# Kernel optimization log

Measured on AMD Instinct MI355X. Metric: run time of the kernel, lower is better.

## Reference

```python
import jax, jax.numpy as jnp
import numpy as np

B, L, D = 2, 2048, 2048
H, HKV, HD = 16, 4, 128
GROUPS = H // HKV


def _rope_tables(key):
    # standard RoPE cos/sin tables, shape (B, L, HD)
    inv_freq = 1.0 / (10000.0 ** (jnp.arange(0, HD, 2, dtype=jnp.float32) / HD))
    pos = jnp.arange(L, dtype=jnp.float32)
    freqs = pos[:, None] * inv_freq[None, :]          # (L, HD/2)
    emb = jnp.concatenate([freqs, freqs], axis=-1)    # (L, HD)
    cos = jnp.broadcast_to(jnp.cos(emb)[None], (B, L, HD))
    sin = jnp.broadcast_to(jnp.sin(emb)[None], (B, L, HD))
    return cos, sin


def setup_inputs() -> dict:
    key = jax.random.key(0)
    ks = jax.random.split(key, 5)
    x = jax.random.normal(ks[0], (B, L, D), dtype=jnp.float32)
    cos, sin = _rope_tables(ks[1])
    s = 1.0 / np.sqrt(D)
    Wq = jax.random.normal(ks[2], (D, D), dtype=jnp.float32) * s
    bq = jnp.zeros((D,), dtype=jnp.float32)
    Wkv = jax.random.normal(ks[3], (2 * HKV * HD, D), dtype=jnp.float32) * s
    bkv = jnp.zeros((2 * HKV * HD,), dtype=jnp.float32)
    Wo = jax.random.normal(ks[4], (D, D), dtype=jnp.float32) * s
    bo = jnp.zeros((D,), dtype=jnp.float32)
    return {"x": x, "cos": cos, "sin": sin, "Wq": Wq, "bq": bq,
            "Wkv": Wkv, "bkv": bkv, "Wo": Wo, "bo": bo}


def _rotate_half(t):
    t1, t2 = jnp.split(t, 2, axis=-1)
    return jnp.concatenate([-t2, t1], axis=-1)


def reference(x, cos, sin, Wq, bq, Wkv, bkv, Wo, bo):
    b, l, d = x.shape
    # QKV projections
    q = (x @ Wq.T + bq).reshape(b, l, H, HD)
    kv = (x @ Wkv.T + bkv).reshape(b, l, 2, HKV, HD)
    k, v = kv[:, :, 0], kv[:, :, 1]
    # RoPE (unsqueeze over head dim, layout B,L,H,D)
    c = cos[:, :, None, :]
    s = sin[:, :, None, :]
    q = q * c + _rotate_half(q) * s
    k = k * c + _rotate_half(k) * s
    # GQA: expand kv heads to query heads
    k = jnp.repeat(k, GROUPS, axis=2)
    v = jnp.repeat(v, GROUPS, axis=2)
    # causal attention (flash_attn_func equivalent math)
    scores = jnp.einsum("blhd,bmhd->bhlm", q, k) / jnp.sqrt(jnp.float32(HD))
    mask = jnp.tril(jnp.ones((l, l), dtype=bool))
    scores = jnp.where(mask[None, None], scores, jnp.finfo(scores.dtype).min)
    attn = jax.nn.softmax(scores, axis=-1)
    out = jnp.einsum("bhlm,bmhd->blhd", attn, v).reshape(b, l, H * HD)
    return out @ Wo.T + bo
```

## Files before the change

kernel.cpp:

```cpp
#include <hip/hip_runtime.h>
#include <hip/hip_bf16.h>
#include <cstddef>

constexpr int B = 2, L = 2048, D = 2048;
constexpr int H = 16, HKV = 4, HD = 128;
constexpr int GROUPS = H / HKV;
constexpr int KVD = 2 * HKV * HD;
constexpr int M_ROWS = B * L;
constexpr int QKVW = D + KVD;

typedef __attribute__((ext_vector_type(8))) short short8;
typedef __attribute__((ext_vector_type(4))) short s16x4;
typedef __attribute__((ext_vector_type(4))) float f32x4;

__device__ __forceinline__ short f2bf(float f) {
    union { float f; unsigned u; } v; v.f = f;
    unsigned r = v.u + 0x7FFFu + ((v.u >> 16) & 1u);
    return (short)(r >> 16);
}

__device__ __forceinline__ float fast_exp2(float x) {
#if __has_builtin(__builtin_amdgcn_exp2f)
    return __builtin_amdgcn_exp2f(x);
#else
    return exp2f(x);
#endif
}

typedef __attribute__((address_space(1))) const void cg_void;
typedef __attribute__((address_space(3))) void lds_void;
__device__ __forceinline__ void gl_lds16(const void* g, void* l) {
    __builtin_amdgcn_global_load_lds((cg_void*)g, (lds_void*)l, 16, 0, 0);
}

__global__ __launch_bounds__(256) void cast_all(
    const float* __restrict__ x, const float* __restrict__ Wq,
    const float* __restrict__ Wkv, const float* __restrict__ Wo,
    short* __restrict__ xb, short* __restrict__ wqkvb, short* __restrict__ wob)
{
    constexpr int n_x   = M_ROWS * D / 4;
    constexpr int n_wq  = D * D / 4;
    constexpr int n_wkv = KVD * D / 4;
    int i = blockIdx.x * 256 + threadIdx.x;
    const float* src; short* dst;
    if (i < n_x)                       { src = x;   dst = xb; }
    else if (i < n_x + n_wq)           { i -= n_x; src = Wq;  dst = wqkvb; }
    else if (i < n_x + n_wq + n_wkv)   { i -= n_x + n_wq; src = Wkv; dst = wqkvb + (size_t)D * D; }
    else                               { i -= n_x + n_wq + n_wkv; src = Wo; dst = wob; }
    const float4 f = ((const float4*)src)[i];
    s16x4 s;
    s[0] = f2bf(f.x); s[1] = f2bf(f.y); s[2] = f2bf(f.z); s[3] = f2bf(f.w);
    ((s16x4*)dst)[i] = s;
}

__global__ __launch_bounds__(256) void bcat(
    const float* __restrict__ bq, const float* __restrict__ bkv, float* __restrict__ o)
{
    const int i = blockIdx.x * 256 + threadIdx.x;
    o[i] = (i < D) ? bq[i] : bkv[i - D];
}

__global__ __launch_bounds__(512, 2) void gemm256(
    const short* __restrict__ Ag, const short* __restrict__ Wg,
    const float* __restrict__ bias, float* __restrict__ C,
    int M, int N, int K)
{
    __shared__ __align__(1024) char smem[131072];

    const int tid = threadIdx.x;
    const int w = tid >> 6, lane = tid & 63;
    const int quad = lane >> 4, n16 = lane & 15;
    const int wr = w >> 2, wc = w & 3;

    const int nbx = gridDim.x;
    const int nwg = nbx * gridDim.y;
    int wg = blockIdx.y * nbx + blockIdx.x;
    wg = (wg & 7) * (nwg >> 3) + (wg >> 3);
    const int bm = (wg / nbx) << 8;
    const int bn = (wg % nbx) << 8;

    const int nkt = K >> 6;

    const int sbo = n16 * 64 + ((quad * 16) ^ ((n16 & 8) << 2));

    const int srow = lane >> 2;
    const int scol = ((lane & 3) * 8) ^ (((lane >> 5) & 1) << 4);

    f32x4 acc[8][4];
#pragma unroll
    for (int i = 0; i < 8; ++i)
#pragma unroll
        for (int j = 0; j < 4; ++j)
#pragma unroll
            for (int r = 0; r < 4; ++r) acc[i][j][r] = 0.f;

    short8 afr[4][2], bfr[2][2];

#define STAGE_A(k0, cb, h)                                                     \
    { _Pragma("unroll") for (int j = 0; j < 2; ++j) {                          \
        const int s  = w + j * 8;                                              \
        const int u  = s >> 1;                                                 \
        const int rg = ((u >> 2) << 3) + ((h) << 2) + (u & 3);                 \
        const int gr = bm + (rg << 4) + srow;                                  \
        const int gc = (k0) + ((s & 1) << 5) + scol;                           \
        gl_lds16(Ag + (size_t)gr * K + gc,                                     \
                 smem + (cb) * 32768 + (h) * 16384 + (s << 10)); } }

#define STAGE_B(k0, cb, h)                                                     \
    { _Pragma("unroll") for (int j = 0; j < 2; ++j) {                          \
        const int s  = w + j * 8;                                              \
        const int u  = s >> 1;                                                 \
        const int rg = ((u >> 1) << 2) + ((h) << 1) + (u & 1);                 \
        const int gr = bn + (rg << 4) + srow;                                  \
        const int gc = (k0) + ((s & 1) << 5) + scol;                           \
        gl_lds16(Wg + (size_t)gr * K + gc,                                     \
                 smem + 65536 + (cb) * 32768 + (h) * 16384 + (s << 10)); } }

#define PHASE(CB, Q, STAGE_STMT, WAIT_STMT)                                    \
    {                                                                          \
        if (((Q) & 1) == 0) {                                                  \
            _Pragma("unroll") for (int mi2 = 0; mi2 < 4; ++mi2)                \
            _Pragma("unroll") for (int kk = 0; kk < 2; ++kk)                   \
                afr[mi2][kk] = *(const short8*)(smem + (CB) * 32768 +          \
                    ((Q) >> 1) * 16384 +                                       \
                    ((((wr * 4 + mi2) * 2) + kk) << 10) + sbo);                \
        }                                                                      \
        _Pragma("unroll") for (int ni2 = 0; ni2 < 2; ++ni2)                    \
        _Pragma("unroll") for (int kk = 0; kk < 2; ++kk)                       \
            bfr[ni2][kk] = *(const short8*)(smem + 65536 + (CB) * 32768 +      \
                ((Q) & 1) * 16384 +                                            \
                ((((wc * 2 + ni2) * 2) + kk) << 10) + sbo);                    \
        STAGE_STMT;                                                            \
        WAIT_STMT;                                                             \
        __builtin_amdgcn_s_barrier();                                          \
        asm volatile("s_waitcnt lgkmcnt(0)" ::: "memory");                     \
        __builtin_amdgcn_sched_barrier(0);                                     \
        __builtin_amdgcn_s_setprio(1);                                         \
        _Pragma("unroll") for (int mi2 = 0; mi2 < 4; ++mi2)                    \
        _Pragma("unroll") for (int ni2 = 0; ni2 < 2; ++ni2)                    \
        _Pragma("unroll") for (int kk = 0; kk < 2; ++kk)                       \
            acc[((Q) >> 1) * 4 + mi2][((Q) & 1) * 2 + ni2] =                   \
                __builtin_amdgcn_mfma_f32_16x16x32_bf16(                       \
                    afr[mi2][kk], bfr[ni2][kk],                                \
                    acc[((Q) >> 1) * 4 + mi2][((Q) & 1) * 2 + ni2], 0, 0, 0);  \
        __builtin_amdgcn_s_setprio(0);                                         \
        asm volatile("" ::: "memory");                                         \
        __builtin_amdgcn_s_barrier();                                          \
    }

#define NOP_WAIT asm volatile("" ::: "memory")

    STAGE_A(0, 0, 0);
    STAGE_B(0, 0, 0);
    STAGE_A(0, 0, 1);
    STAGE_B(0, 0, 1);
    if (nkt > 1) {
        STAGE_A(64, 1, 0);
        STAGE_B(64, 1, 0);
    }
    asm volatile("s_waitcnt vmcnt(4)" ::: "memory");
    __builtin_amdgcn_s_barrier();

    for (int t = 0; t < nkt; t += 2) {
        const int k1 = (t + 1) << 6, k2 = (t + 2) << 6, k3 = (t + 3) << 6;
        const bool g2 = (t + 2) < nkt, g3 = (t + 3) < nkt;

        PHASE(0, 0, { STAGE_A(k1, 1, 1); }, NOP_WAIT);
        PHASE(0, 1, { STAGE_B(k1, 1, 1); }, NOP_WAIT);
        PHASE(0, 2, { if (g2) STAGE_A(k2, 0, 0); }, NOP_WAIT);
        PHASE(0, 3, { if (g2) STAGE_B(k2, 0, 0); },
              { if (g2) asm volatile("s_waitcnt vmcnt(4)" ::: "memory");
                else    asm volatile("s_waitcnt vmcnt(0)" ::: "memory"); });

        PHASE(1, 0, { if (g2) STAGE_A(k2, 0, 1); }, NOP_WAIT);
        PHASE(1, 1, { if (g2) STAGE_B(k2, 0, 1); }, NOP_WAIT);
        PHASE(1, 2, { if (g3) STAGE_A(k3, 1, 0); }, NOP_WAIT);
        PHASE(1, 3, { if (g3) STAGE_B(k3, 1, 0); },
              { if (g3) asm volatile("s_waitcnt vmcnt(4)" ::: "memory");
                else    asm volatile("s_waitcnt vmcnt(0)" ::: "memory"); });
    }

#undef PHASE
#undef STAGE_A
#undef STAGE_B
#undef NOP_WAIT

#pragma unroll
    for (int mh = 0; mh < 2; ++mh)
#pragma unroll
        for (int mi2 = 0; mi2 < 4; ++mi2)
#pragma unroll
            for (int r = 0; r < 4; ++r) {
                const int row = bm + wr * 128 + mh * 64 + mi2 * 16 + quad * 4 + r;
#pragma unroll
                for (int nh = 0; nh < 2; ++nh)
#pragma unroll
                    for (int ni2 = 0; ni2 < 2; ++ni2) {
                        const int col = bn + wc * 64 + nh * 32 + ni2 * 16 + n16;
                        C[(size_t)row * N + col] =
                            acc[mh * 4 + mi2][nh * 2 + ni2][r] + bias[col];
                    }
            }
}

__global__ __launch_bounds__(256) void rope_bf(
    const float* __restrict__ qkv, const float* __restrict__ cosp,
    const float* __restrict__ sinp, short* __restrict__ qb, short* __restrict__ kb)
{
    const int row = blockIdx.x;
    const int tid = threadIdx.x;
    const int b = row / L, l = row % L;
    const float* cr = cosp + (size_t)row * HD;
    const float* sr = sinp + (size_t)row * HD;
    const float* base = qkv + (size_t)row * QKVW;

    for (int p = tid; p < H * 64; p += 256) {
        const int h = p >> 6, i = p & 63;
        const float* qr = base + h * HD;
        short* qo = qb + (size_t)row * D + h * HD;
        const float t1 = qr[i], t2 = qr[i + 64];
        qo[i]      = f2bf(t1 * cr[i]      - t2 * sr[i]);
        qo[i + 64] = f2bf(t2 * cr[i + 64] + t1 * sr[i + 64]);
    }
    {
        const int h = tid >> 6, i = tid & 63;
        const float* krow = base + D + h * HD;
        short* ko = kb + ((size_t)(b * HKV + h) * L + l) * HD;
        const float t1 = krow[i], t2 = krow[i + 64];
        ko[i]      = f2bf(t1 * cr[i]      - t2 * sr[i]);
        ko[i + 64] = f2bf(t2 * cr[i + 64] + t1 * sr[i + 64]);
    }
}

__global__ __launch_bounds__(256) void vt_kernel(
    const float* __restrict__ qkv, short* __restrict__ vt)
{
    __shared__ short T[32][72];
    const int lt = blockIdx.x, dt = blockIdx.y, bh = blockIdx.z;
    const int b = bh >> 2, hkv = bh & 3;
    const int tid = threadIdx.x;

#pragma unroll
    for (int pass = 0; pass < 2; ++pass) {
        const int ll = pass * 32 + (tid >> 3);
        const int dl = (tid & 7) * 4;
        const int l = lt * 64 + ll;
        const float4 f = *(const float4*)&qkv[
            ((size_t)(b * L + l)) * QKVW + D + HKV * HD + hkv * HD + dt * 32 + dl];
        T[dl + 0][ll] = f2bf(f.x); T[dl + 1][ll] = f2bf(f.y);
        T[dl + 2][ll] = f2bf(f.z); T[dl + 3][ll] = f2bf(f.w);
    }
    __syncthreads();
#pragma unroll
    for (int pass = 0; pass < 2; ++pass) {
        const int dl = pass * 16 + (tid >> 4);
        const int l4 = (tid & 15) * 4;
        const int d = dt * 32 + dl;
        *(s16x4*)&vt[((size_t)bh * HD + d) * L + lt * 64 + l4] = *(const s16x4*)&T[dl][l4];
    }
}

__global__ __launch_bounds__(512) void attn_mfma4(
    const short* __restrict__ qb_, const short* __restrict__ kb_,
    const short* __restrict__ vtb_, short* __restrict__ ob)
{
    __shared__ __align__(16) char smem[86016];
    short* const KsB  = (short*)smem;
    short* const VtB  = (short*)(smem + 32768);
    short* const PbB  = (short*)(smem + 65536);
    float* const Rbuf = (float*)smem;

    const int hkv = blockIdx.y, b = blockIdx.z;
    const int tid = threadIdx.x;
    const int w = tid >> 6, lane = tid & 63;
    const int quad = lane >> 4, n16 = lane & 15;
    const int h   = hkv * GROUPS + (w & 3);
    const int kh  = (w >> 2) * 32;
    const int khg = (w >> 2) * 4;

    const size_t kbase  = (size_t)(b * HKV + hkv) * L * HD;
    const size_t vtbase = (size_t)(b * HKV + hkv) * HD * L;
    const float c1 = 0.12751845f;
    const float c0 = -28.853901f;

    short8 ones;
#pragma unroll
    for (int i = 0; i < 8; ++i) ones[i] = (short)0x3F80;

    const int kr = lane >> 4;
    const int kg_sw = lane & 15;
    const int vr = lane >> 3;
    const int vg_sw = lane & 7;

    short* const myPb = PbB + w * (2 * 16 * 40);

#pragma unroll 1
    for (int phase = 0; phase < 2; ++phase) {
        const int qidx = phase ? (63 - (int)blockIdx.x) : (int)blockIdx.x;
        const int qb0 = qidx * 32;
        const int ntiles = (qidx >> 1) + 1;

        short8 qf[2][4];
#pragma unroll
        for (int rt = 0; rt < 2; ++rt)
#pragma unroll
            for (int kk = 0; kk < 4; ++kk)
                qf[rt][kk] = *(const short8*)&qb_[
                    ((size_t)(b * L + qb0 + rt * 16 + n16)) * D + h * HD + kk * 32 + quad * 8];

        f32x4 oacc[2][8], lacc[2];
#pragma unroll
        for (int rt = 0; rt < 2; ++rt) {
#pragma unroll
            for (int r = 0; r < 4; ++r) lacc[rt][r] = 0.f;
#pragma unroll
            for (int nt = 0; nt < 8; ++nt)
#pragma unroll
                for (int r = 0; r < 4; ++r) oacc[rt][nt][r] = 0.f;
        }

        __syncthreads();

        {
            const short* kg = kb_ + kbase;
            const short* vg = vtb_ + vtbase;
#pragma unroll
            for (int j = 0; j < 2; ++j) {
                const int chunk = w * 2 + j;
                const int r = chunk * 4 + kr;
                gl_lds16(kg + r * HD + (kg_sw ^ (r & 15)) * 8, KsB + chunk * 512);
            }
#pragma unroll
            for (int j = 0; j < 2; ++j) {
                const int chunk = w * 2 + j;
                const int d = chunk * 8 + vr;
                gl_lds16(vg + (size_t)d * L + (vg_sw ^ (d & 7)) * 8, VtB + chunk * 512);
            }
        }

        for (int kt = 0; kt < ntiles; ++kt) {
            const int buf = kt & 1;
            __syncthreads();

            if (kt + 1 < ntiles) {
                const short* kg = kb_ + kbase + (size_t)((kt + 1) * 64) * HD;
                const short* vg = vtb_ + vtbase + (kt + 1) * 64;
#pragma unroll
                for (int j = 0; j < 2; ++j) {
                    const int chunk = w * 2 + j;
                    const int r = chunk * 4 + kr;
                    gl_lds16(kg + r * HD + (kg_sw ^ (r & 15)) * 8,
                             KsB + (buf ^ 1) * 8192 + chunk * 512);
                }
#pragma unroll
                for (int j = 0; j < 2; ++j) {
                    const int chunk = w * 2 + j;
                    const int d = chunk * 8 + vr;
                    gl_lds16(vg + (size_t)d * L + (vg_sw ^ (d & 7)) * 8,
                             VtB + (buf ^ 1) * 8192 + chunk * 512);
                }
            }

            const short* Ks = KsB + buf * 8192;
            const short* Vt = VtB + buf * 8192;

            f32x4 s[2][2];
#pragma unroll
            for (int rt = 0; rt < 2; ++rt)
#pragma unroll
                for (int ktl = 0; ktl < 2; ++ktl)
#pragma unroll
                    for (int r = 0; r < 4; ++r) s[rt][ktl][r] = 0.f;
#pragma unroll
            for (int kk = 0; kk < 4; ++kk) {
                short8 kf[2];
#pragma unroll
                for (int ktl = 0; ktl < 2; ++ktl) {
                    const int row = kh + ktl * 16 + n16;
                    kf[ktl] = *(const short8*)&Ks[row * 128 + ((kk * 4 + quad) ^ n16) * 8];
                }
#pragma unroll
                for (int rt = 0; rt < 2; ++rt)
#pragma unroll
                    for (int ktl = 0; ktl < 2; ++ktl)
                        s[rt][ktl] = __builtin_amdgcn_mfma_f32_16x16x32_bf16(
                            qf[rt][kk], kf[ktl], s[rt][ktl], 0, 0, 0);
            }

            const bool lastt = (kt == ntiles - 1);
#pragma unroll
            for (int rt = 0; rt < 2; ++rt) {
#pragma unroll
                for (int ktl = 0; ktl < 2; ++ktl) {
                    const int key0 = kt * 64 + kh + ktl * 16 + n16;
#pragma unroll
                    for (int r = 0; r < 4; ++r) {
                        float sv = s[rt][ktl][r];
                        if (lastt) {
                            const int qi = qb0 + rt * 16 + quad * 4 + r;
                            sv = (key0 <= qi) ? sv : -1e30f;
                        }
                        const float e = fast_exp2(sv * c1 + c0);
                        myPb[(rt * 16 + quad * 4 + r) * 40 + ktl * 16 + n16] = f2bf(e);
                    }
                }
            }
            asm volatile("s_waitcnt lgkmcnt(0)" ::: "memory");

            short8 pf[2];
#pragma unroll
            for (int rt = 0; rt < 2; ++rt)
                pf[rt] = *(const short8*)&myPb[(rt * 16 + n16) * 40 + quad * 8];
#pragma unroll
            for (int rt = 0; rt < 2; ++rt)
                lacc[rt] = __builtin_amdgcn_mfma_f32_16x16x32_bf16(pf[rt], ones, lacc[rt], 0, 0, 0);
#pragma unroll
            for (int nt = 0; nt < 8; ++nt) {
                const short8 vf = *(const short8*)&Vt[
                    (nt * 16 + n16) * 64 + ((khg + quad) ^ (n16 & 7)) * 8];
#pragma unroll
                for (int rt = 0; rt < 2; ++rt)
                    oacc[rt][nt] = __builtin_amdgcn_mfma_f32_16x16x32_bf16(pf[rt], vf, oacc[rt][nt], 0, 0, 0);
            }
        }

        __syncthreads();
        if (w >= 4) {
            float* rp = Rbuf + ((size_t)(w - 4) * 64 + lane) * 76;
#pragma unroll
            for (int rt = 0; rt < 2; ++rt)
#pragma unroll
                for (int nt = 0; nt < 8; ++nt)
                    *(f32x4*)&rp[(rt * 8 + nt) * 4] = oacc[rt][nt];
            *(f32x4*)&rp[64] = lacc[0];
            *(f32x4*)&rp[68] = lacc[1];
        }
        __syncthreads();
        if (w < 4) {
            const float* rp = Rbuf + ((size_t)w * 64 + lane) * 76;
#pragma unroll
            for (int rt = 0; rt < 2; ++rt) {
                const f32x4 lr = *(const f32x4*)&rp[64 + rt * 4];
#pragma unroll
                for (int r = 0; r < 4; ++r) lacc[rt][r] += lr[r];
#pragma unroll
                for (int nt = 0; nt < 8; ++nt) {
                    const f32x4 o2 = *(const f32x4*)&rp[(rt * 8 + nt) * 4];
#pragma unroll
                    for (int r = 0; r < 4; ++r) oacc[rt][nt][r] += o2[r];
                }
            }
#pragma unroll
            for (int rt = 0; rt < 2; ++rt) {
#pragma unroll
                for (int r = 0; r < 4; ++r) {
                    const float inv = 1.0f / lacc[rt][r];
                    short* op = ob + ((size_t)(b * L + qb0 + rt * 16 + quad * 4 + r)) * D + h * HD + n16;
#pragma unroll
                    for (int nt = 0; nt < 8; ++nt) op[nt * 16] = f2bf(oacc[rt][nt][r] * inv);
                }
            }
        }
    }
}

extern "C" void kernel_launch(void* const* d_in, const int* in_sizes, int n_in,
                              void* d_out, int out_size, void* d_ws, size_t ws_size,
                              hipStream_t stream)
{
    const float* x    = (const float*)d_in[0];
    const float* cosp = (const float*)d_in[1];
    const float* sinp = (const float*)d_in[2];
    const float* Wq   = (const float*)d_in[3];
    const float* bq   = (const float*)d_in[4];
    const float* Wkv  = (const float*)d_in[5];
    const float* bkv  = (const float*)d_in[6];
    const float* Wo   = (const float*)d_in[7];
    const float* bo   = (const float*)d_in[8];
    float* out = (float*)d_out;

    char* p = (char*)d_ws;
    float* qkv_ws = (float*)p; p += (size_t)M_ROWS * QKVW * 4;
    short* x_bf    = (short*)p; p += (size_t)M_ROWS * D * 2;
    short* wqkv_bf = (short*)p; p += (size_t)QKVW * D * 2;
    short* wo_bf   = (short*)p; p += (size_t)D * D * 2;
    float* b_qkv   = (float*)p; p += (size_t)QKVW * 4;
    short* q_bf    = (short*)p; p += (size_t)M_ROWS * D * 2;
    short* k_bf    = (short*)p; p += (size_t)M_ROWS * HKV * HD * 2;
    short* vt_bf   = (short*)p;
    short* attn_bf = x_bf;

    dim3 blk(256);

    cast_all<<<dim3(18432), blk, 0, stream>>>(x, Wq, Wkv, Wo, x_bf, wqkv_bf, wo_bf);
    bcat<<<dim3(QKVW / 256), blk, 0, stream>>>(bq, bkv, b_qkv);

    gemm256<<<dim3(QKVW / 256, M_ROWS / 256), dim3(512), 0, stream>>>(
        x_bf, wqkv_bf, b_qkv, qkv_ws, M_ROWS, QKVW, D);

    rope_bf<<<dim3(M_ROWS), blk, 0, stream>>>(qkv_ws, cosp, sinp, q_bf, k_bf);
    vt_kernel<<<dim3(L / 64, HD / 32, B * HKV), blk, 0, stream>>>(qkv_ws, vt_bf);

    attn_mfma4<<<dim3(32, HKV, B), dim3(512), 0, stream>>>(q_bf, k_bf, vt_bf, attn_bf);

    gemm256<<<dim3(D / 256, M_ROWS / 256), dim3(512), 0, stream>>>(
        attn_bf, wo_bf, bo, out, M_ROWS, D, D);
}
```

Baseline: 319.1 us.

## Fuse RoPE and V-transpose into QKV GEMM epilogue via permuted weight rows

Permutes the rows of Wq, the K half of Wkv and their biases during the bf16 cast so that each lane's accumulator holds both RoPE partner elements (i and i+64). The QKV GEMM epilogue can then apply RoPE directly and write bf16 Q and K, and write V transposed in bf16. This removes the fp32 QKV workspace round trip and the separate rope and transpose kernels. The cost is a heavier epilogue that reads cos/sin per row and does scattered 2-byte and strided stores.

```diff
diff --git a/kernel.cpp b/kernel.cpp
--- a/kernel.cpp
+++ b/kernel.cpp
@@ -25,6 +25,11 @@
 #else
     return exp2f(x);
 #endif
+}
+
+__device__ __forceinline__ int invp(int pos) {
+    const int b16 = pos >> 4, j = pos & 15;
+    return ((b16 >> 1) << 4) + j + ((b16 & 1) << 6);
 }
 
 typedef __attribute__((address_space(1))) const void cg_void;
@@ -41,13 +46,28 @@
     constexpr int n_x   = M_ROWS * D / 4;
     constexpr int n_wq  = D * D / 4;
     constexpr int n_wkv = KVD * D / 4;
+    constexpr int RPW   = D / 4;
     int i = blockIdx.x * 256 + threadIdx.x;
-    const float* src; short* dst;
-    if (i < n_x)                       { src = x;   dst = xb; }
-    else if (i < n_x + n_wq)           { i -= n_x; src = Wq;  dst = wqkvb; }
-    else if (i < n_x + n_wq + n_wkv)   { i -= n_x + n_wq; src = Wkv; dst = wqkvb + (size_t)D * D; }
-    else                               { i -= n_x + n_wq + n_wkv; src = Wo; dst = wob; }
-    const float4 f = ((const float4*)src)[i];
+    const float* src; short* dst; int isrc;
+    if (i < n_x) {
+        src = x; dst = xb; isrc = i;
+    } else if (i < n_x + n_wq) {
+        i -= n_x; src = Wq; dst = wqkvb;
+        const int fi = i / RPW, col = i % RPW;
+        const int head = fi >> 7, pos = fi & 127;
+        isrc = ((head << 7) + invp(pos)) * RPW + col;
+    } else if (i < n_x + n_wq + n_wkv) {
+        i -= n_x + n_wq; src = Wkv; dst = wqkvb + (size_t)D * D;
+        const int fi = i / RPW, col = i % RPW;
+        if (fi < HKV * HD) {
+            isrc = (((fi >> 7) << 7) + invp(fi & 127)) * RPW + col;
+        } else {
+            isrc = i;
+        }
+    } else {
+        i -= n_x + n_wq + n_wkv; src = Wo; dst = wob; isrc = i;
+    }
+    const float4 f = ((const float4*)src)[isrc];
     s16x4 s;
     s[0] = f2bf(f.x); s[1] = f2bf(f.y); s[2] = f2bf(f.z); s[3] = f2bf(f.w);
     ((s16x4*)dst)[i] = s;
@@ -57,12 +77,19 @@
     const float* __restrict__ bq, const float* __restrict__ bkv, float* __restrict__ o)
 {
     const int i = blockIdx.x * 256 + threadIdx.x;
-    o[i] = (i < D) ? bq[i] : bkv[i - D];
-}
-
+    float v;
+    if (i < D)                  v = bq[((i >> 7) << 7) + invp(i & 127)];
+    else if (i < D + HKV * HD)  v = bkv[(((i - D) >> 7) << 7) + invp((i - D) & 127)];
+    else                        v = bkv[i - D];
+    o[i] = v;
+}
+
+template<int MODE>
 __global__ __launch_bounds__(512, 2) void gemm256(
     const short* __restrict__ Ag, const short* __restrict__ Wg,
     const float* __restrict__ bias, float* __restrict__ C,
+    const float* __restrict__ cosp, const float* __restrict__ sinp,
+    short* __restrict__ qout, short* __restrict__ kout, short* __restrict__ vtout,
     int M, int N, int K)
 {
     __shared__ __align__(1024) char smem[131072];
@@ -185,78 +212,78 @@
 #undef STAGE_B
 #undef NOP_WAIT
 
-#pragma unroll
-    for (int mh = 0; mh < 2; ++mh)
-#pragma unroll
-        for (int mi2 = 0; mi2 < 4; ++mi2)
-#pragma unroll
-            for (int r = 0; r < 4; ++r) {
-                const int row = bm + wr * 128 + mh * 64 + mi2 * 16 + quad * 4 + r;
+    if (MODE == 0) {
+#pragma unroll
+        for (int mh = 0; mh < 2; ++mh)
+#pragma unroll
+            for (int mi2 = 0; mi2 < 4; ++mi2)
+#pragma unroll
+                for (int r = 0; r < 4; ++r) {
+                    const int row = bm + wr * 128 + mh * 64 + mi2 * 16 + quad * 4 + r;
+#pragma unroll
+                    for (int nh = 0; nh < 2; ++nh)
+#pragma unroll
+                        for (int ni2 = 0; ni2 < 2; ++ni2) {
+                            const int col = bn + wc * 64 + nh * 32 + ni2 * 16 + n16;
+                            C[(size_t)row * N + col] =
+                                acc[mh * 4 + mi2][nh * 2 + ni2][r] + bias[col];
+                        }
+                }
+    } else if (bn < D + HKV * HD) {
+        const bool isK = (bn >= D);
+#pragma unroll
+        for (int mh = 0; mh < 2; ++mh)
+#pragma unroll
+            for (int mi2 = 0; mi2 < 4; ++mi2)
+#pragma unroll
+                for (int r = 0; r < 4; ++r) {
+                    const int row = bm + wr * 128 + mh * 64 + mi2 * 16 + quad * 4 + r;
+                    const float* csrow = cosp + (size_t)row * HD;
+                    const float* snrow = sinp + (size_t)row * HD;
+#pragma unroll
+                    for (int nh = 0; nh < 2; ++nh) {
+                        const int c_lo = bn + wc * 64 + nh * 32 + n16;
+                        const int iif  = (wc & 1) * 32 + nh * 16 + n16;
+                        const float a  = acc[mh * 4 + mi2][nh * 2 + 0][r] + bias[c_lo];
+                        const float bb = acc[mh * 4 + mi2][nh * 2 + 1][r] + bias[c_lo + 16];
+                        const float olo = a * csrow[iif]       - bb * snrow[iif];
+                        const float ohi = bb * csrow[iif + 64] + a * snrow[iif + 64];
+                        if (!isK) {
+                            short* qp = qout + (size_t)row * D + c_lo;
+                            qp[0]  = f2bf(olo);
+                            qp[16] = f2bf(ohi);
+                        } else {
+                            const int ck = c_lo - D;
+                            const int hk = ck >> 7, dk = ck & 127;
+                            const int b_ = row >> 11, l_ = row & (L - 1);
+                            short* kp = kout + ((size_t)(b_ * HKV + hk) * L + l_) * HD + dk;
+                            kp[0]  = f2bf(olo);
+                            kp[16] = f2bf(ohi);
+                        }
+                    }
+                }
+    } else {
+#pragma unroll
+        for (int mh = 0; mh < 2; ++mh)
+#pragma unroll
+            for (int mi2 = 0; mi2 < 4; ++mi2) {
+                const int row0 = bm + wr * 128 + mh * 64 + mi2 * 16 + quad * 4;
+                const int b_ = row0 >> 11, l_ = row0 & (L - 1);
 #pragma unroll
                 for (int nh = 0; nh < 2; ++nh)
 #pragma unroll
                     for (int ni2 = 0; ni2 < 2; ++ni2) {
-                        const int col = bn + wc * 64 + nh * 32 + ni2 * 16 + n16;
-                        C[(size_t)row * N + col] =
-                            acc[mh * 4 + mi2][nh * 2 + ni2][r] + bias[col];
+                        const int c  = bn + wc * 64 + nh * 32 + ni2 * 16 + n16;
+                        const int cv = c - (D + HKV * HD);
+                        const int hv = cv >> 7, dv = cv & 127;
+                        const float bs = bias[c];
+                        s16x4 sv;
+#pragma unroll
+                        for (int r = 0; r < 4; ++r)
+                            sv[r] = f2bf(acc[mh * 4 + mi2][nh * 2 + ni2][r] + bs);
+                        *(s16x4*)&vtout[((size_t)(b_ * HKV + hv) * HD + dv) * L + l_] = sv;
                     }
             }
-}
-
-__global__ __launch_bounds__(256) void rope_bf(
-    const float* __restrict__ qkv, const float* __restrict__ cosp,
-    const float* __restrict__ sinp, short* __restrict__ qb, short* __restrict__ kb)
-{
-    const int row = blockIdx.x;
-    const int tid = threadIdx.x;
-    const int b = row / L, l = row % L;
-    const float* cr = cosp + (size_t)row * HD;
-    const float* sr = sinp + (size_t)row * HD;
-    const float* base = qkv + (size_t)row * QKVW;
-
-    for (int p = tid; p < H * 64; p += 256) {
-        const int h = p >> 6, i = p & 63;
-        const float* qr = base + h * HD;
-        short* qo = qb + (size_t)row * D + h * HD;
-        const float t1 = qr[i], t2 = qr[i + 64];
-        qo[i]      = f2bf(t1 * cr[i]      - t2 * sr[i]);
-        qo[i + 64] = f2bf(t2 * cr[i + 64] + t1 * sr[i + 64]);
-    }
-    {
-        const int h = tid >> 6, i = tid & 63;
-        const float* krow = base + D + h * HD;
-        short* ko = kb + ((size_t)(b * HKV + h) * L + l) * HD;
-        const float t1 = krow[i], t2 = krow[i + 64];
-        ko[i]      = f2bf(t1 * cr[i]      - t2 * sr[i]);
-        ko[i + 64] = f2bf(t2 * cr[i + 64] + t1 * sr[i + 64]);
-    }
-}
-
-__global__ __launch_bounds__(256) void vt_kernel(
-    const float* __restrict__ qkv, short* __restrict__ vt)
-{
-    __shared__ short T[32][72];
-    const int lt = blockIdx.x, dt = blockIdx.y, bh = blockIdx.z;
-    const int b = bh >> 2, hkv = bh & 3;
-    const int tid = threadIdx.x;
-
-#pragma unroll
-    for (int pass = 0; pass < 2; ++pass) {
-        const int ll = pass * 32 + (tid >> 3);
-        const int dl = (tid & 7) * 4;
-        const int l = lt * 64 + ll;
-        const float4 f = *(const float4*)&qkv[
-            ((size_t)(b * L + l)) * QKVW + D + HKV * HD + hkv * HD + dt * 32 + dl];
-        T[dl + 0][ll] = f2bf(f.x); T[dl + 1][ll] = f2bf(f.y);
-        T[dl + 2][ll] = f2bf(f.z); T[dl + 3][ll] = f2bf(f.w);
-    }
-    __syncthreads();
-#pragma unroll
-    for (int pass = 0; pass < 2; ++pass) {
-        const int dl = pass * 16 + (tid >> 4);
-        const int l4 = (tid & 15) * 4;
-        const int d = dt * 32 + dl;
-        *(s16x4*)&vt[((size_t)bh * HD + d) * L + lt * 64 + l4] = *(const s16x4*)&T[dl][l4];
     }
 }
 
@@ -480,7 +507,6 @@
     float* out = (float*)d_out;
 
     char* p = (char*)d_ws;
-    float* qkv_ws = (float*)p; p += (size_t)M_ROWS * QKVW * 4;
     short* x_bf    = (short*)p; p += (size_t)M_ROWS * D * 2;
     short* wqkv_bf = (short*)p; p += (size_t)QKVW * D * 2;
     short* wo_bf   = (short*)p; p += (size_t)D * D * 2;
@@ -495,14 +521,13 @@
     cast_all<<<dim3(18432), blk, 0, stream>>>(x, Wq, Wkv, Wo, x_bf, wqkv_bf, wo_bf);
     bcat<<<dim3(QKVW / 256), blk, 0, stream>>>(bq, bkv, b_qkv);
 
-    gemm256<<<dim3(QKVW / 256, M_ROWS / 256), dim3(512), 0, stream>>>(
-        x_bf, wqkv_bf, b_qkv, qkv_ws, M_ROWS, QKVW, D);
-
-    rope_bf<<<dim3(M_ROWS), blk, 0, stream>>>(qkv_ws, cosp, sinp, q_bf, k_bf);
-    vt_kernel<<<dim3(L / 64, HD / 32, B * HKV), blk, 0, stream>>>(qkv_ws, vt_bf);
+    gemm256<1><<<dim3(QKVW / 256, M_ROWS / 256), dim3(512), 0, stream>>>(
+        x_bf, wqkv_bf, b_qkv, nullptr, cosp, sinp, q_bf, k_bf, vt_bf,
+        M_ROWS, QKVW, D);
 
     attn_mfma4<<<dim3(32, HKV, B), dim3(512), 0, stream>>>(q_bf, k_bf, vt_bf, attn_bf);
 
-    gemm256<<<dim3(D / 256, M_ROWS / 256), dim3(512), 0, stream>>>(
-        attn_bf, wo_bf, bo, out, M_ROWS, D, D);
-}
+    gemm256<0><<<dim3(D / 256, M_ROWS / 256), dim3(512), 0, stream>>>(
+        attn_bf, wo_bf, bo, out, nullptr, nullptr, nullptr, nullptr, nullptr,
+        M_ROWS, D, D);
+}
```

Measured after the change: 328.0 us. +2.8%, slower.
